# Kernel tuning notes

Measured on AMD Instinct MI355X. Metric: run time of the kernel, lower is better.

The kernel has to match this reference:

```python
import jax, jax.numpy as jnp
import numpy as np

DIM = 64; N_LAYER = 2; B = 2048; M = 64
N_ENT = 100000; N_REL = 200
TEMP = 0.2; KGE_W = 1e-6
MIN_N = 1e-15; BND = 1e-5


def _norm(x):
    return jnp.sqrt(jnp.clip((x * x).sum(-1, keepdims=True), MIN_N))


def _l2(x):
    # F.normalize(p=2): x / max(||x||, 1e-12)
    return x / jnp.maximum(jnp.sqrt((x * x).sum(-1, keepdims=True)), 1e-12)


def _artanh(x):
    return jnp.arctanh(jnp.clip(x, -1.0 + BND, 1.0 - BND))


def expmap0(u):
    n = _norm(u)
    return jnp.tanh(n) * u / n


def logmap0(x):
    n = _norm(x)
    return _artanh(n) * x / n


def mobius_add(x, y):
    x2 = (x * x).sum(-1, keepdims=True)
    y2 = (y * y).sum(-1, keepdims=True)
    xy = (x * y).sum(-1, keepdims=True)
    num = (1 + 2 * xy + y2) * x + (1 - x2) * y
    den = 1 + 2 * xy + x2 * y2
    return num / jnp.clip(den, MIN_N)


def expmap(u, p):
    lam = 2.0 / jnp.clip(1.0 - (p * p).sum(-1, keepdims=True), MIN_N)
    n = _norm(u)
    return mobius_add(p, jnp.tanh(lam * n / 2.0) * u / n)


def logmap(x, p):
    m = mobius_add(-p, x)
    n = _norm(m)
    lam = 2.0 / jnp.clip(1.0 - (p * p).sum(-1, keepdims=True), MIN_N)
    return (2.0 / lam) * _artanh(n) * m / n


def _ed_agg(h, path, t, att_w1, att_w2):
    # attention: Linear(2d,d,no bias) -> LeakyReLU(0)==ReLU -> Linear(d,1,no bias) -> Sigmoid
    x = jnp.concatenate([h, path], -1)                       # [B,M,2d]
    a = jax.nn.sigmoid(jax.nn.relu(x @ att_w1) @ att_w2)[..., 0]  # [B,M]
    w = jax.nn.softmax(a, axis=-1)
    return (w[..., None] * t).sum(1)                          # [B,d]


def _hyper_agg(h, path, t, curvature, a2_w1, a2_b1, a2_w2, a2_b2):
    h, path, t = _l2(h), _l2(path), _l2(t)
    hh = expmap0(h) * jnp.abs(curvature)
    ht = expmap(t, hh)
    hr = expmap(path, hh)
    tang = logmap0(jnp.concatenate([hh, hr], -1))            # [B,M,2d]
    a = jnp.tanh(jax.nn.relu(tang @ a2_w1 + a2_b1) @ a2_w2 + a2_b2)[..., 0]
    w = jax.nn.softmax(a, axis=-1)                            # [B,M]
    agg = w[..., None] * ht
    mean_pt = (w[..., None] * hh).sum(1, keepdims=True)       # [B,1,d]
    e = logmap(agg, mean_pt)
    return (w[..., None] * e).sum(1)                          # [B,d]


def _build(E, R, h_idx, r_idx, t_idx, init_emb, agg):
    embs = [init_emb]
    for i in range(N_LAYER):
        h = E[h_idx[0]]
        path = R[r_idx[0]]
        for k in range(1, i + 1):  # faithful to source: inner loop reuses index i
            h = h + E[h_idx[i]]
            path = path * R[r_idx[i]]
        embs.append(agg(h, path, E[t_idx[i]]))
    return jnp.stack(embs)  # [L+1, B, d]


def _mlcl(a_stack, b_stack):
    # vectorized over layer index i of MLCL_Loss(a[i], b[i], a_list, b_list)
    na, nb = _l2(a_stack), _l2(b_stack)                       # [L+1,B,d]
    d = na.shape[-1]
    pos = (na * nb).sum(-1)                                   # [L+1,B]
    ttl1 = jnp.einsum('lbd,md->lbm', na, nb.reshape(-1, d))
    ttl2 = jnp.einsum('lbd,md->lbm', nb, na.reshape(-1, d))
    ep = jnp.exp(pos / TEMP)
    l1 = -jnp.log(ep / jnp.exp(ttl1 / TEMP).sum(-1)).sum()
    l2 = -jnp.log(ep / jnp.exp(ttl2 / TEMP).sum(-1)).sum()
    return KGE_W * (l1 + l2)


def _cat_rev(stack):
    # e = stack[0]; for i in 1..L: e = cat(stack[i], e) -> [L, L-1, ..., 0]
    return jnp.concatenate([stack[i] for i in range(stack.shape[0] - 1, -1, -1)], -1)


def setup_inputs() -> dict:
    key = jax.random.key(0)
    ks = jax.random.split(key, 24)
    def ent_idx(k):
        return jax.random.randint(k, (N_LAYER, B, M), 0, N_ENT, dtype=jnp.int32)
    def rel_idx(k):
        return jax.random.randint(k, (N_LAYER, B, M), 0, N_REL, dtype=jnp.int32)
    inp = {
        'items': jax.random.randint(ks[0], (B,), 0, N_ENT, dtype=jnp.int32),
        'ucf_h': ent_idx(ks[1]), 'ucf_r': rel_idx(ks[2]), 'ucf_t': ent_idx(ks[3]),
        'ikg_h': ent_idx(ks[4]), 'ikg_r': rel_idx(ks[5]), 'ikg_t': ent_idx(ks[6]),
        'ukg_h': ent_idx(ks[7]), 'ukg_r': rel_idx(ks[8]), 'ukg_t': ent_idx(ks[9]),
        'icf_h': ent_idx(ks[10]), 'icf_r': rel_idx(ks[11]), 'icf_t': ent_idx(ks[12]),
        'ent_emb': jax.random.normal(ks[13], (N_ENT, DIM), jnp.float32) * 0.02,
        'rel_emb': jax.random.normal(ks[14], (N_REL, DIM), jnp.float32) * 0.02,
        'att_w1': jax.random.normal(ks[15], (2 * DIM, DIM), jnp.float32) * 0.05,
        'att_w2': jax.random.normal(ks[16], (DIM, 1), jnp.float32) * 0.05,
        'att2_w1': jax.random.normal(ks[17], (2 * DIM, DIM), jnp.float32) * 0.05,
        'att2_b1': jnp.zeros((DIM,), jnp.float32),
        'att2_w2': jax.random.normal(ks[18], (DIM, 1), jnp.float32) * 0.05,
        'att2_b2': jnp.zeros((1,), jnp.float32),
        'curvature': jnp.asarray(1.0, jnp.float32),
    }
    return inp


def reference(items, ucf_h, ucf_r, ucf_t, ikg_h, ikg_r, ikg_t,
              ukg_h, ukg_r, ukg_t, icf_h, icf_r, icf_t,
              ent_emb, rel_emb, att_w1, att_w2,
              att2_w1, att2_b1, att2_w2, att2_b2, curvature):
    ed = lambda h, p, t: _ed_agg(h, p, t, att_w1, att_w2)
    hy = lambda h, p, t: _hyper_agg(h, p, t, curvature, att2_w1, att2_b1, att2_w2, att2_b2)
    ucf = _build(ent_emb, rel_emb, ucf_h, ucf_r, ucf_t, ent_emb[ucf_h[0]].mean(1), ed)
    ikg = _build(ent_emb, rel_emb, ikg_h, ikg_r, ikg_t, ent_emb[items], ed)
    ukg = _build(ent_emb, rel_emb, ukg_h, ukg_r, ukg_t, ent_emb[ukg_h[0]].mean(1), hy)
    icf = _build(ent_emb, rel_emb, icf_h, icf_r, icf_t, ent_emb[icf_h[0]].mean(1), hy)
    kge_loss = _mlcl(ucf, ukg) + _mlcl(ikg, icf)
    e_u = jnp.concatenate([_cat_rev(ucf), _cat_rev(ukg)], -1)
    e_i = jnp.concatenate([_cat_rev(icf), _cat_rev(ikg)], -1)
    scores = jax.nn.sigmoid((e_i * e_u).sum(-1))
    return scores, kge_loss
```

## Files before the change

kernel.cpp:

```cpp
#include <hip/hip_runtime.h>
#include <hip/hip_bf16.h>
#include <cstdint>
#include <cstddef>

constexpr int NB = 2048;
constexpr int NM = 64;
constexpr int ND = 64;
constexpr int NBM = NB * NM;
constexpr int NROWS = 3 * NB;
constexpr int STACK = 3 * NB * ND;
constexpr int NZ = 8;

typedef __attribute__((ext_vector_type(8))) short short8;
typedef __attribute__((ext_vector_type(4))) float float4v;

__device__ __forceinline__ float wsum(float v) {
#pragma unroll
  for (int o = 32; o > 0; o >>= 1) v += __shfl_xor(v, o, 64);
  return v;
}

__device__ __forceinline__ float wmax(float v) {
#pragma unroll
  for (int o = 32; o > 0; o >>= 1) v = fmaxf(v, __shfl_xor(v, o, 64));
  return v;
}

__device__ __forceinline__ float rcpf(float x) { return __builtin_amdgcn_rcpf(x); }
__device__ __forceinline__ float sqf(float x) { return __builtin_amdgcn_sqrtf(x); }

__device__ __forceinline__ float fast_tanh(float x) {
  float t = __expf(2.f * x);
  return (t - 1.f) * rcpf(t + 1.f);
}

__device__ __forceinline__ float artanh_clip(float x) {
  x = fminf(fmaxf(x, -1.f + 1e-5f), 1.f - 1e-5f);
  return 0.5f * __logf((1.f + x) * rcpf(1.f - x));
}

__device__ __forceinline__ ushort f2bf(float f) {
  return (ushort)((__float_as_uint(f) + 0x8000u) >> 16);
}
__device__ __forceinline__ float bf2f(ushort u) {
  return __uint_as_float((uint)u << 16);
}
__device__ __forceinline__ uint pack_bf2(float h, float p) {
  uint hu = __float_as_uint(h) + 0x8000u;
  uint pu = __float_as_uint(p) + 0x8000u;
  return __builtin_amdgcn_perm(pu, hu, 0x07060302);
}
__device__ __forceinline__ float hp_lo(uint v) { return __uint_as_float(v << 16); }
__device__ __forceinline__ float hp_hi(uint v) { return __uint_as_float(v & 0xFFFF0000u); }

__device__ __forceinline__ float readlane_f(float v, int l) {
  return __int_as_float(__builtin_amdgcn_readlane(__float_as_int(v), l));
}

__device__ __forceinline__ void write_row_norm(
    float v, float* __restrict__ frow, ushort* __restrict__ nstack,
    int r, int lane) {
  float nv = wsum(v * v);
  float rr = rcpf(fmaxf(sqf(nv), 1e-12f));
  frow[lane] = v;
  int q = (lane >> 3) & 3, half = lane >> 5, j = lane & 7;
  int fl = (r & 15) | (q << 4);
  nstack[(size_t)(r >> 4) * 1024 + fl * 16 + half * 8 + j] = f2bf(v * rr);
}

__global__ __launch_bounds__(64) void prep_kernel(
    const float* __restrict__ E, const int* __restrict__ items,
    const float* __restrict__ w1_ed, const float* __restrict__ w1_hy,
    float* __restrict__ s_ikg, ushort* __restrict__ nbf_ikg,
    ushort* __restrict__ w1p_ed, ushort* __restrict__ w1p_hy) {
  int blk = blockIdx.x, lane = threadIdx.x;
  if (blk < NB) {
    float v = E[(size_t)items[blk] * ND + lane];
    write_row_norm(v, s_ikg + (size_t)blk * ND, nbf_ikg, blk, lane);
  } else {
    int e = (blk - NB) * 64 + lane;
    const float* w1 = (e < 8192) ? w1_ed : w1_hy;
    ushort* out = (e < 8192) ? w1p_ed : w1p_hy;
    e &= 8191;
    int j = e & 7, ln = (e >> 3) & 63, nt = (e >> 9) & 3, kt = e >> 11;
    int n = nt * 16 + (ln & 15), k = kt * 32 + ((ln >> 4) << 3) + j;
    out[e] = f2bf(w1[k * 64 + n]);
  }
}

constexpr int OFF_H = 0;
constexpr int OFF_P = 4608;
constexpr int OFF_T = 9728;
constexpr int XS = 152;
constexpr int REGA_SZ = 14336;

__global__ __launch_bounds__(256) void agg_all_kernel(
    const float* __restrict__ E, const float* __restrict__ R,
    const int* __restrict__ h0, const int* __restrict__ r0, const int* __restrict__ t0,
    const int* __restrict__ h1, const int* __restrict__ r1, const int* __restrict__ t1,
    const int* __restrict__ h2, const int* __restrict__ r2, const int* __restrict__ t2,
    const int* __restrict__ h3, const int* __restrict__ r3, const int* __restrict__ t3,
    const ushort* __restrict__ w1p_ed, const float* __restrict__ w2_ed,
    const ushort* __restrict__ w1p_hy, const float* __restrict__ b1,
    const float* __restrict__ w2_hy, const float* __restrict__ b2,
    const float* __restrict__ curv,
    float* __restrict__ stacks, ushort* __restrict__ nbf) {
  __shared__ __align__(16) ushort regA[REGA_SZ];
  __shared__ float a_s[64];
  __shared__ float part[4][64];
  __shared__ float minit[4][64];

  const int b = blockIdx.x;
  const int fam = blockIdx.y;
  const int tid = threadIdx.x;
  const int wave = tid >> 6, lane = tid & 63;
  const int m0 = __builtin_amdgcn_readfirstlane(wave) * 16;
  const int colq = lane & 15, quad = lane >> 4;
  const size_t L = (size_t)NB * ND;

  const int* h_idx = (fam == 0) ? h0 : (fam == 1) ? h1 : (fam == 2) ? h2 : h3;
  const int* r_idx = (fam == 0) ? r0 : (fam == 1) ? r1 : (fam == 2) ? r2 : r3;
  const int* t_idx = (fam == 0) ? t0 : (fam == 1) ? t1 : (fam == 2) ? t2 : t3;
  float* sb = stacks + (size_t)fam * STACK;
  ushort* nb = nbf + (size_t)fam * STACK;

  uint hp[16];

  if (fam < 2) {
    const int do_init = (fam == 0);
    for (int layer = 0; layer < 2; ++layer) {
      float tv[16];
      if (layer == 0) {
        float macc = 0.f;
#pragma unroll
        for (int mi = 0; mi < 16; ++mi) {
          const int m = m0 + mi;
          float hd = E[(size_t)h_idx[b * NM + m] * ND + lane];
          float pd = R[(size_t)r_idx[b * NM + m] * ND + lane];
          macc += hd;
          uint pk = pack_bf2(hd, pd);
          hp[mi] = pk;
          regA[m * XS + lane] = (ushort)pk;
          regA[m * XS + 64 + lane] = (ushort)(pk >> 16);
        }
        if (do_init) minit[wave][lane] = macc;
      } else {
#pragma unroll
        for (int mi = 0; mi < 16; ++mi) {
          const int m = m0 + mi;
          float hd = hp_lo(hp[mi]) + E[(size_t)h_idx[NBM + b * NM + m] * ND + lane];
          float pd = hp_hi(hp[mi]) * R[(size_t)r_idx[NBM + b * NM + m] * ND + lane];
          uint pk = pack_bf2(hd, pd);
          hp[mi] = pk;
          regA[m * XS + lane] = (ushort)pk;
          regA[m * XS + 64 + lane] = (ushort)(pk >> 16);
        }
      }
#pragma unroll
      for (int mi = 0; mi < 16; ++mi)
        tv[mi] = E[(size_t)t_idx[(size_t)layer * NBM + b * NM + m0 + mi] * ND + lane];

      {
        short8 afr[4];
#pragma unroll
        for (int kt = 0; kt < 4; ++kt)
          afr[kt] = *(const short8*)&regA[(m0 + colq) * XS + kt * 32 + quad * 8];
        float w2v[4];
#pragma unroll
        for (int nt = 0; nt < 4; ++nt) w2v[nt] = w2_ed[nt * 16 + colq];
        float cc[4][4];
#pragma unroll
        for (int nt = 0; nt < 4; ++nt) {
          float4v c = {0.f, 0.f, 0.f, 0.f};
#pragma unroll
          for (int kt = 0; kt < 4; ++kt) {
            short8 bfr = *(const short8*)&w1p_ed[(((kt << 2) | nt) * 64 + lane) * 8];
            c = __builtin_amdgcn_mfma_f32_16x16x32_bf16(afr[kt], bfr, c, 0, 0, 0);
          }
#pragma unroll
          for (int i = 0; i < 4; ++i) cc[nt][i] = c[i];
        }
        float sred[4];
#pragma unroll
        for (int i = 0; i < 4; ++i)
          sred[i] = fmaxf(cc[0][i], 0.f) * w2v[0] + fmaxf(cc[1][i], 0.f) * w2v[1] +
                    fmaxf(cc[2][i], 0.f) * w2v[2] + fmaxf(cc[3][i], 0.f) * w2v[3];
#pragma unroll
        for (int o = 8; o > 0; o >>= 1) {
#pragma unroll
          for (int i = 0; i < 4; ++i) sred[i] += __shfl_xor(sred[i], o, 64);
        }
        if (colq == 0) {
#pragma unroll
          for (int i = 0; i < 4; ++i)
            a_s[m0 + quad * 4 + i] = 1.f / (1.f + __expf(-sred[i]));
        }
      }
      __syncthreads();

      float wl;
      {
        float v = a_s[lane];
        float mx = wmax(v);
        float e = __expf(v - mx);
        wl = e / wsum(e);
      }
      if (layer == 0 && do_init && wave == 0) {
        float v = (minit[0][lane] + minit[1][lane] + minit[2][lane] + minit[3][lane]) * (1.f / 64.f);
        write_row_norm(v, sb + (size_t)b * ND, nb, b, lane);
      }

      float o = 0.f;
#pragma unroll
      for (int mi = 0; mi < 16; ++mi)
        o = fmaf(readlane_f(wl, m0 + mi), tv[mi], o);
      part[wave][lane] = o;
      __syncthreads();
      if (wave == 0) {
        float v = part[0][lane] + part[1][lane] + part[2][lane] + part[3][lane];
        write_row_norm(v, sb + (layer + 1) * L + (size_t)b * ND,
                       nb, (layer + 1) * NB + b, lane);
      }
    }
  } else {
    const float cabs = fabsf(*curv);
    const int j = colq;
    const int srcl = ((j >> 2) << 4) + j;

    for (int layer = 0; layer < 2; ++layer) {
      if (layer == 0) {
        float macc = 0.f;
#pragma unroll
        for (int mi = 0; mi < 16; ++mi) {
          const int m = m0 + mi;
          float hd = E[(size_t)h_idx[b * NM + m] * ND + lane];
          float pd = R[(size_t)r_idx[b * NM + m] * ND + lane];
          float td = E[(size_t)t_idx[b * NM + m] * ND + lane];
          macc += hd;
          uint pk = pack_bf2(hd, pd);
          hp[mi] = pk;
          regA[OFF_H + m * 72 + lane] = (ushort)pk;
          regA[OFF_P + m * 72 + lane] = (ushort)(pk >> 16);
          regA[OFF_T + m * 72 + lane] = f2bf(td);
        }
        part[wave][lane] = macc;
      } else {
#pragma unroll
        for (int mi = 0; mi < 16; ++mi) {
          const int m = m0 + mi;
          float hd = hp_lo(hp[mi]) + E[(size_t)h_idx[NBM + b * NM + m] * ND + lane];
          float pd = hp_hi(hp[mi]) * R[(size_t)r_idx[NBM + b * NM + m] * ND + lane];
          float td = E[(size_t)t_idx[(size_t)NBM + b * NM + m] * ND + lane];
          uint pk = pack_bf2(hd, pd);
          hp[mi] = pk;
          regA[OFF_H + m * 72 + lane] = (ushort)pk;
          regA[OFF_P + m * 72 + lane] = (ushort)(pk >> 16);
          regA[OFF_T + m * 72 + lane] = f2bf(td);
        }
      }

      float sh, sp, st, sht, shp;
      {
        const int fr = m0 + colq;
        const ushort* pH = &regA[OFF_H + fr * 72 + quad * 8];
        const ushort* pP = &regA[OFF_P + fr * 72 + quad * 8];
        const ushort* pT = &regA[OFF_T + fr * 72 + quad * 8];
        short8 hh0 = *(const short8*)pH, hh1 = *(const short8*)(pH + 32);
        short8 pp0 = *(const short8*)pP, pp1 = *(const short8*)(pP + 32);
        short8 tt0 = *(const short8*)pT, tt1 = *(const short8*)(pT + 32);
        const int dr = colq & 3;
#define DIAG_DOT(OUTV, A0, A1, B0, B1)                                      \
        {                                                                    \
          float4v c = {0.f, 0.f, 0.f, 0.f};                                  \
          c = __builtin_amdgcn_mfma_f32_16x16x32_bf16(A0, B0, c, 0, 0, 0);   \
          c = __builtin_amdgcn_mfma_f32_16x16x32_bf16(A1, B1, c, 0, 0, 0);   \
          float dv = (dr & 2) ? ((dr & 1) ? c[3] : c[2])                     \
                              : ((dr & 1) ? c[1] : c[0]);                    \
          OUTV = __shfl(dv, srcl, 64);                                       \
        }
        DIAG_DOT(sh, hh0, hh1, hh0, hh1)
        DIAG_DOT(sp, pp0, pp1, pp0, pp1)
        DIAG_DOT(st, tt0, tt1, tt0, tt1)
        DIAG_DOT(sht, hh0, hh1, tt0, tt1)
        DIAG_DOT(shp, hh0, hh1, pp0, pp1)
#undef DIAG_DOT
      }

      float g_ch, g_e1, g_e2, g_gh, g_q1, g_q2, g_hts2;
      {
        float rih = rcpf(fmaxf(sqf(sh), 1e-12f));
        float rip = rcpf(fmaxf(sqf(sp), 1e-12f));
        float rit = rcpf(fmaxf(sqf(st), 1e-12f));
        float nh = sqf(fmaxf(sh * rih * rih, 1e-15f));
        float ch = fast_tanh(nh) * rcpf(nh) * rih * cabs;
        float p2 = ch * ch * sh;
        float lam = 2.f * rcpf(fmaxf(1.f - p2, 1e-15f));
        float ntn = sqf(fmaxf(st * rit * rit, 1e-15f));
        float ct = fast_tanh(0.5f * lam * ntn) * rcpf(ntn) * rit;
        float y2 = ct * ct * st, xy = ch * ct * sht;
        float At = 1.f + 2.f * xy + y2, Bt = 1.f - p2;
        float rdt = rcpf(fmaxf(1.f + 2.f * xy + p2 * y2, 1e-15f));
        g_e1 = At * ch * rdt;
        g_e2 = Bt * ct * rdt;
        g_hts2 = g_e1 * g_e1 * sh + 2.f * g_e1 * g_e2 * sht + g_e2 * g_e2 * st;
        float npn = sqf(fmaxf(sp * rip * rip, 1e-15f));
        float cp = fast_tanh(0.5f * lam * npn) * rcpf(npn) * rip;
        float z2 = cp * cp * sp, xz = ch * cp * shp;
        float Ar = 1.f + 2.f * xz + z2;
        float rdr = rcpf(fmaxf(1.f + 2.f * xz + p2 * z2, 1e-15f));
        float f1 = Ar * ch * rdr, f2 = Bt * cp * rdr;
        float hr2 = f1 * f1 * sh + 2.f * f1 * f2 * shp + f2 * f2 * sp;
        float n128 = sqf(fmaxf(p2 + hr2, 1e-15f));
        float fq = artanh_clip(n128) * rcpf(n128);
        g_ch = ch;
        g_gh = fq * ch;
        g_q1 = fq * f1;
        g_q2 = fq * f2;
      }

      __syncthreads();
      if (layer == 0 && wave == 0) {
        float v = (part[0][lane] + part[1][lane] + part[2][lane] + part[3][lane]) * (1.f / 64.f);
        write_row_norm(v, sb + (size_t)b * ND, nb, b, lane);
      }

#pragma unroll
      for (int mi = 0; mi < 16; ++mi) {
        const int m = m0 + mi;
        float hvf = hp_lo(hp[mi]);
        float pvf = hp_hi(hp[mi]);
        float tvf = bf2f(regA[OFF_T + m * 72 + lane]);
        float ghm = readlane_f(g_gh, mi);
        float q1m = readlane_f(g_q1, mi);
        float q2m = readlane_f(g_q2, mi);
        float e1m = readlane_f(g_e1, mi);
        float e2m = readlane_f(g_e2, mi);
        regA[m * XS + lane] = f2bf(ghm * hvf);
        regA[m * XS + 64 + lane] = f2bf(q1m * hvf + q2m * pvf);
        regA[OFF_T + m * 72 + lane] = f2bf(e1m * hvf + e2m * tvf);
      }

      {
        short8 afr[4];
#pragma unroll
        for (int kt = 0; kt < 4; ++kt)
          afr[kt] = *(const short8*)&regA[(m0 + colq) * XS + kt * 32 + quad * 8];
        float b1v[4], w2v[4];
#pragma unroll
        for (int nt = 0; nt < 4; ++nt) {
          b1v[nt] = b1[nt * 16 + colq];
          w2v[nt] = w2_hy[nt * 16 + colq];
        }
        float cc[4][4];
#pragma unroll
        for (int nt = 0; nt < 4; ++nt) {
          float4v c = {0.f, 0.f, 0.f, 0.f};
#pragma unroll
          for (int kt = 0; kt < 4; ++kt) {
            short8 bfr = *(const short8*)&w1p_hy[(((kt << 2) | nt) * 64 + lane) * 8];
            c = __builtin_amdgcn_mfma_f32_16x16x32_bf16(afr[kt], bfr, c, 0, 0, 0);
          }
#pragma unroll
          for (int i = 0; i < 4; ++i) cc[nt][i] = c[i];
        }
        float b2v = b2[0];
        float sred[4];
#pragma unroll
        for (int i = 0; i < 4; ++i)
          sred[i] = fmaxf(cc[0][i] + b1v[0], 0.f) * w2v[0] +
                    fmaxf(cc[1][i] + b1v[1], 0.f) * w2v[1] +
                    fmaxf(cc[2][i] + b1v[2], 0.f) * w2v[2] +
                    fmaxf(cc[3][i] + b1v[3], 0.f) * w2v[3];
#pragma unroll
        for (int o = 8; o > 0; o >>= 1) {
#pragma unroll
          for (int i = 0; i < 4; ++i) sred[i] += __shfl_xor(sred[i], o, 64);
        }
        if (colq == 0) {
#pragma unroll
          for (int i = 0; i < 4; ++i)
            a_s[m0 + quad * 4 + i] = fast_tanh(sred[i] + b2v);
        }
      }
      __syncthreads();

      float wl;
      {
        float v = a_s[lane];
        float mx = wmax(v);
        float e = __expf(v - mx);
        wl = e / wsum(e);
      }

      float mp = 0.f;
#pragma unroll
      for (int mi = 0; mi < 16; ++mi)
        mp = fmaf(readlane_f(wl, m0 + mi) * readlane_f(g_ch, mi), hp_lo(hp[mi]), mp);
      part[wave][lane] = mp;
      __syncthreads();

      float mv = part[0][lane] + part[1][lane] + part[2][lane] + part[3][lane];
      float p2m = wsum(mv * mv);

      float dpv;
      {
        const ushort* pA = &regA[OFF_T + (m0 + colq) * 72 + quad * 8];
        short8 a0 = *(const short8*)pA, a1 = *(const short8*)(pA + 32);
        short8 bm0, bm1;
#pragma unroll
        for (int jj = 0; jj < 8; ++jj) {
          bm0[jj] = (short)f2bf(__shfl(mv, quad * 8 + jj, 64));
          bm1[jj] = (short)f2bf(__shfl(mv, 32 + quad * 8 + jj, 64));
        }
        float4v c = {0.f, 0.f, 0.f, 0.f};
        c = __builtin_amdgcn_mfma_f32_16x16x32_bf16(a0, bm0, c, 0, 0, 0);
        c = __builtin_amdgcn_mfma_f32_16x16x32_bf16(a1, bm1, c, 0, 0, 0);
        const int dr = colq & 3;
        float dv = (dr & 2) ? ((dr & 1) ? c[3] : c[2]) : ((dr & 1) ? c[1] : c[0]);
        dpv = __shfl(dv, srcl, 64);
      }

      const float be = fmaxf(1.f - p2m, 1e-15f);
      float g1, g2;
      {
        float wm = __shfl(wl, m0 + j, 64);
        float y2 = wm * wm * g_hts2;
        float xy = -wm * dpv;
        float al = 1.f + 2.f * xy + y2;
        float rd = rcpf(fmaxf(1.f + 2.f * xy + p2m * y2, 1e-15f));
        float md2 = (al * al * p2m - 2.f * al * be * wm * dpv + be * be * y2) * rd * rd;
        float n = sqf(fmaxf(md2, 1e-15f));
        float sm = be * artanh_clip(n) * rcpf(n) * rd;
        g1 = wm * wm * sm * be;
        g2 = wm * sm * al;
      }
      float ovec = 0.f, cA = 0.f;
#pragma unroll
      for (int mi = 0; mi < 16; ++mi) {
        const int m = m0 + mi;
        float htf = bf2f(regA[OFF_T + m * 72 + lane]);
        ovec = fmaf(readlane_f(g1, mi), htf, ovec);
        cA += readlane_f(g2, mi);
      }
      part[wave][lane] = ovec - cA * mv;
      __syncthreads();
      if (wave == 0) {
        float v = part[0][lane] + part[1][lane] + part[2][lane] + part[3][lane];
        write_row_norm(v, sb + (layer + 1) * L + (size_t)b * ND,
                       nb, (layer + 1) * NB + b, lane);
      }
    }
  }
}

__global__ __launch_bounds__(256) void pos_scores_kernel(
    const ushort* __restrict__ nbf, const float* __restrict__ stacks,
    float* __restrict__ pos, float* __restrict__ out) {
  int lane = threadIdx.x & 63;
  int wave = threadIdx.x >> 6;
  if (blockIdx.y < 2) {
    if (blockIdx.x >= 96) return;
    int g = blockIdx.x * 4 + wave;
    int sa = blockIdx.y;
    const ushort* X = nbf + (size_t)sa * STACK + (size_t)g * 1024 + lane * 16;
    const ushort* Yp = nbf + (size_t)(sa + 2) * STACK + (size_t)g * 1024 + lane * 16;
    short8 x0 = *(const short8*)X, x1 = *(const short8*)(X + 8);
    short8 y0 = *(const short8*)Yp, y1 = *(const short8*)(Yp + 8);
    float d = 0.f;
#pragma unroll
    for (int jj = 0; jj < 8; ++jj)
      d += bf2f((ushort)x0[jj]) * bf2f((ushort)y0[jj]) +
           bf2f((ushort)x1[jj]) * bf2f((ushort)y1[jj]);
    d += __shfl_xor(d, 16, 64);
    d += __shfl_xor(d, 32, 64);
    if (lane < 16) pos[sa * NROWS + g * 16 + lane] = d;
  } else {
    int b = blockIdx.x * 4 + wave;
    if (b >= NB) return;
    float s = 0.f;
#pragma unroll
    for (int l = 0; l < 3; ++l) {
      size_t o = (size_t)l * NB * ND + (size_t)b * ND + lane;
      s += stacks[0 * (size_t)STACK + o] * stacks[3 * (size_t)STACK + o]
         + stacks[2 * (size_t)STACK + o] * stacks[1 * (size_t)STACK + o];
    }
    s = wsum(s);
    if (lane == 0) out[b] = 1.f / (1.f + __expf(-s));
  }
}

__global__ __launch_bounds__(256) void lse_mfma_kernel(
    const ushort* __restrict__ nbf, float* __restrict__ Spart) {
  const int tid = threadIdx.x;
  const int wave = tid >> 6, lane = tid & 63;
  const int pair = blockIdx.y;
  const int z = blockIdx.z;
  int xi = (pair & 2) ? ((pair & 1) ? 3 : 1) : ((pair & 1) ? 2 : 0);
  int yi = xi ^ 2;
  const ushort* X = nbf + (size_t)xi * STACK;
  const ushort* Y = nbf + (size_t)yi * STACK;
  const int r0 = blockIdx.x * 64 + wave * 16;
  const int g = r0 >> 4;
  const int row = lane & 15, quad = lane >> 4;
  (void)quad;

  short8 a0 = *(const short8*)&X[(size_t)g * 1024 + lane * 16];
  short8 a1 = *(const short8*)&X[(size_t)g * 1024 + lane * 16 + 8];

  float rsum[4] = {0.f, 0.f, 0.f, 0.f};
  const int cg0 = z * (NROWS / NZ / 16);
  for (int ct = 0; ct < NROWS / NZ / 16; ++ct) {
    const ushort* yp = &Y[(size_t)(cg0 + ct) * 1024 + lane * 16];
    short8 b0 = *(const short8*)yp;
    short8 b1 = *(const short8*)(yp + 8);
    float4v c = {0.f, 0.f, 0.f, 0.f};
    c = __builtin_amdgcn_mfma_f32_16x16x32_bf16(a0, b0, c, 0, 0, 0);
    c = __builtin_amdgcn_mfma_f32_16x16x32_bf16(a1, b1, c, 0, 0, 0);
#pragma unroll
    for (int i = 0; i < 4; ++i) rsum[i] += __expf(c[i] * 5.f);
  }
#pragma unroll
  for (int i = 0; i < 4; ++i) {
    float v = rsum[i];
    v += __shfl_xor(v, 1, 64);
    v += __shfl_xor(v, 2, 64);
    v += __shfl_xor(v, 4, 64);
    v += __shfl_xor(v, 8, 64);
    if (row == 0)
      Spart[((size_t)z * 4 + pair) * NROWS + r0 + (lane >> 4) * 4 + i] = v;
  }
}

__global__ __launch_bounds__(256) void loss_part_kernel(
    const float* __restrict__ Spart, const float* __restrict__ pos,
    double* __restrict__ lossp) {
  __shared__ double red[256];
  const int t = threadIdx.x, blk = blockIdx.x;
  double acc = 0.0;
#pragma unroll
  for (int r = 0; r < 2; ++r) {
    int i = blk * 512 + r * 256 + t;
    float s = 0.f;
#pragma unroll
    for (int zz = 0; zz < NZ; ++zz) s += Spart[i + zz * 4 * NROWS];
    acc += (double)__logf(s);
  }
  {
    int jj = blk * 256 + t;
    acc -= 10.0 * (double)pos[jj];
  }
  red[t] = acc;
  __syncthreads();
  for (int s = 128; s > 0; s >>= 1) {
    if (t < s) red[t] += red[t + s];
    __syncthreads();
  }
  if (t == 0) lossp[blk] = red[0];
}

__global__ __launch_bounds__(64) void loss_final_kernel(
    const double* __restrict__ lossp, float* __restrict__ out) {
  int lane = threadIdx.x;
  double v = (lane < 48) ? lossp[lane] : 0.0;
#pragma unroll
  for (int o = 32; o > 0; o >>= 1) v += __shfl_xor(v, o, 64);
  if (lane == 0) out[NB] = (float)(1e-6 * v);
}

extern "C" void kernel_launch(void* const* d_in, const int* in_sizes, int n_in,
                              void* d_out, int out_size, void* d_ws, size_t ws_size,
                              hipStream_t stream) {
  const int* items = (const int*)d_in[0];
  const int* ucf_h = (const int*)d_in[1];
  const int* ucf_r = (const int*)d_in[2];
  const int* ucf_t = (const int*)d_in[3];
  const int* ikg_h = (const int*)d_in[4];
  const int* ikg_r = (const int*)d_in[5];
  const int* ikg_t = (const int*)d_in[6];
  const int* ukg_h = (const int*)d_in[7];
  const int* ukg_r = (const int*)d_in[8];
  const int* ukg_t = (const int*)d_in[9];
  const int* icf_h = (const int*)d_in[10];
  const int* icf_r = (const int*)d_in[11];
  const int* icf_t = (const int*)d_in[12];
  const float* E = (const float*)d_in[13];
  const float* R = (const float*)d_in[14];
  const float* att_w1 = (const float*)d_in[15];
  const float* att_w2 = (const float*)d_in[16];
  const float* a2_w1 = (const float*)d_in[17];
  const float* a2_b1 = (const float*)d_in[18];
  const float* a2_w2 = (const float*)d_in[19];
  const float* a2_b2 = (const float*)d_in[20];
  const float* curv = (const float*)d_in[21];
  float* outp = (float*)d_out;

  float* ws = (float*)d_ws;
  float* stacks = ws;
  float* Spart = stacks + 4 * (size_t)STACK;
  float* posarr = Spart + (size_t)NZ * 4 * NROWS;
  ushort* nbf = (ushort*)(posarr + 2 * (size_t)NROWS);
  ushort* w1p_ed = nbf + 4 * (size_t)STACK;
  ushort* w1p_hy = w1p_ed + 8192;
  double* lossp = (double*)(w1p_hy + 8192);

  float* ikg = stacks + 1 * (size_t)STACK;
  ushort* nbf_ikg = nbf + 1 * (size_t)STACK;

  prep_kernel<<<NB + 256, 64, 0, stream>>>(E, items, att_w1, a2_w1,
                                           ikg, nbf_ikg, w1p_ed, w1p_hy);

  agg_all_kernel<<<dim3(NB, 4), 256, 0, stream>>>(
      E, R,
      ucf_h, ucf_r, ucf_t, ikg_h, ikg_r, ikg_t,
      ukg_h, ukg_r, ukg_t, icf_h, icf_r, icf_t,
      w1p_ed, att_w2, w1p_hy, a2_b1, a2_w2, a2_b2, curv,
      stacks, nbf);

  pos_scores_kernel<<<dim3(NB / 4, 3), 256, 0, stream>>>(nbf, stacks, posarr, outp);
  lse_mfma_kernel<<<dim3(NROWS / 64, 4, NZ), 256, 0, stream>>>(nbf, Spart);

  loss_part_kernel<<<48, 256, 0, stream>>>(Spart, posarr, lossp);
  loss_final_kernel<<<1, 64, 0, stream>>>(lossp, outp);
}
```

Before: 385.3 us.

## Write normalized rows row-major and relayout to MFMA fragments in separate kernel

The aggregation kernel now stores each normalized bf16 row contiguously instead of scattering it into the MFMA fragment layout. A new relayout kernel copies these rows into a separate fragment-ordered buffer, which the LSE MFMA kernel reads. The positive-pair dot kernel is rewritten to use the row-major copy with one wave per row and a full wave reduction. The aim is simpler, coalesced stores in the main kernel, at the cost of an extra launch, an extra workspace buffer and one more pass over the bf16 stacks.

```diff
diff --git a/kernel.cpp b/kernel.cpp
--- a/kernel.cpp
+++ b/kernel.cpp
@@ -58,14 +58,11 @@
 }
 
 __device__ __forceinline__ void write_row_norm(
-    float v, float* __restrict__ frow, ushort* __restrict__ nstack,
-    int r, int lane) {
+    float v, float* __restrict__ frow, ushort* __restrict__ nrow, int lane) {
   float nv = wsum(v * v);
-  float rr = rcpf(fmaxf(sqf(nv), 1e-12f));
+  float r = rcpf(fmaxf(sqf(nv), 1e-12f));
   frow[lane] = v;
-  int q = (lane >> 3) & 3, half = lane >> 5, j = lane & 7;
-  int fl = (r & 15) | (q << 4);
-  nstack[(size_t)(r >> 4) * 1024 + fl * 16 + half * 8 + j] = f2bf(v * rr);
+  nrow[lane] = f2bf(v * r);
 }
 
 __global__ __launch_bounds__(64) void prep_kernel(
@@ -76,7 +73,7 @@
   int blk = blockIdx.x, lane = threadIdx.x;
   if (blk < NB) {
     float v = E[(size_t)items[blk] * ND + lane];
-    write_row_norm(v, s_ikg + (size_t)blk * ND, nbf_ikg, blk, lane);
+    write_row_norm(v, s_ikg + (size_t)blk * ND, nbf_ikg + (size_t)blk * ND, lane);
   } else {
     int e = (blk - NB) * 64 + lane;
     const float* w1 = (e < 8192) ? w1_ed : w1_hy;
@@ -207,7 +204,7 @@
       }
       if (layer == 0 && do_init && wave == 0) {
         float v = (minit[0][lane] + minit[1][lane] + minit[2][lane] + minit[3][lane]) * (1.f / 64.f);
-        write_row_norm(v, sb + (size_t)b * ND, nb, b, lane);
+        write_row_norm(v, sb + (size_t)b * ND, nb + (size_t)b * ND, lane);
       }
 
       float o = 0.f;
@@ -219,7 +216,7 @@
       if (wave == 0) {
         float v = part[0][lane] + part[1][lane] + part[2][lane] + part[3][lane];
         write_row_norm(v, sb + (layer + 1) * L + (size_t)b * ND,
-                       nb, (layer + 1) * NB + b, lane);
+                       nb + (layer + 1) * L + (size_t)b * ND, lane);
       }
     }
   } else {
@@ -321,7 +318,7 @@
       __syncthreads();
       if (layer == 0 && wave == 0) {
         float v = (part[0][lane] + part[1][lane] + part[2][lane] + part[3][lane]) * (1.f / 64.f);
-        write_row_norm(v, sb + (size_t)b * ND, nb, b, lane);
+        write_row_norm(v, sb + (size_t)b * ND, nb + (size_t)b * ND, lane);
       }
 
 #pragma unroll
@@ -447,10 +444,22 @@
       if (wave == 0) {
         float v = part[0][lane] + part[1][lane] + part[2][lane] + part[3][lane];
         write_row_norm(v, sb + (layer + 1) * L + (size_t)b * ND,
-                       nb, (layer + 1) * NB + b, lane);
+                       nb + (layer + 1) * L + (size_t)b * ND, lane);
       }
     }
   }
+}
+
+__global__ __launch_bounds__(256) void relayout_kernel(
+    const ushort* __restrict__ nbf, ushort* __restrict__ nbfF) {
+  int lane = threadIdx.x & 63;
+  int wave = threadIdx.x >> 6;
+  int g = blockIdx.x * 4 + wave;
+  int s = blockIdx.y;
+  const ushort* src = nbf + (size_t)s * STACK + (size_t)(g * 16 + (lane & 15)) * ND + (lane >> 4) * 8;
+  ushort* dst = nbfF + (size_t)s * STACK + (size_t)g * 1024 + lane * 16;
+  *(short8*)dst = *(const short8*)src;
+  *(short8*)(dst + 8) = *(const short8*)(src + 32);
 }
 
 __global__ __launch_bounds__(256) void pos_scores_kernel(
@@ -459,21 +468,12 @@
   int lane = threadIdx.x & 63;
   int wave = threadIdx.x >> 6;
   if (blockIdx.y < 2) {
-    if (blockIdx.x >= 96) return;
-    int g = blockIdx.x * 4 + wave;
+    int row = blockIdx.x * 4 + wave;
     int sa = blockIdx.y;
-    const ushort* X = nbf + (size_t)sa * STACK + (size_t)g * 1024 + lane * 16;
-    const ushort* Yp = nbf + (size_t)(sa + 2) * STACK + (size_t)g * 1024 + lane * 16;
-    short8 x0 = *(const short8*)X, x1 = *(const short8*)(X + 8);
-    short8 y0 = *(const short8*)Yp, y1 = *(const short8*)(Yp + 8);
-    float d = 0.f;
-#pragma unroll
-    for (int jj = 0; jj < 8; ++jj)
-      d += bf2f((ushort)x0[jj]) * bf2f((ushort)y0[jj]) +
-           bf2f((ushort)x1[jj]) * bf2f((ushort)y1[jj]);
-    d += __shfl_xor(d, 16, 64);
-    d += __shfl_xor(d, 32, 64);
-    if (lane < 16) pos[sa * NROWS + g * 16 + lane] = d;
+    float a = bf2f(nbf[(size_t)sa * STACK + (size_t)row * ND + lane]);
+    float c = bf2f(nbf[(size_t)(sa + 2) * STACK + (size_t)row * ND + lane]);
+    float d = wsum(a * c);
+    if (lane == 0) pos[sa * NROWS + row] = d;
   } else {
     int b = blockIdx.x * 4 + wave;
     if (b >= NB) return;
@@ -490,19 +490,18 @@
 }
 
 __global__ __launch_bounds__(256) void lse_mfma_kernel(
-    const ushort* __restrict__ nbf, float* __restrict__ Spart) {
+    const ushort* __restrict__ nbfF, float* __restrict__ Spart) {
   const int tid = threadIdx.x;
   const int wave = tid >> 6, lane = tid & 63;
   const int pair = blockIdx.y;
   const int z = blockIdx.z;
   int xi = (pair & 2) ? ((pair & 1) ? 3 : 1) : ((pair & 1) ? 2 : 0);
   int yi = xi ^ 2;
-  const ushort* X = nbf + (size_t)xi * STACK;
-  const ushort* Y = nbf + (size_t)yi * STACK;
+  const ushort* X = nbfF + (size_t)xi * STACK;
+  const ushort* Y = nbfF + (size_t)yi * STACK;
   const int r0 = blockIdx.x * 64 + wave * 16;
   const int g = r0 >> 4;
-  const int row = lane & 15, quad = lane >> 4;
-  (void)quad;
+  const int row = lane & 15;
 
   short8 a0 = *(const short8*)&X[(size_t)g * 1024 + lane * 16];
   short8 a1 = *(const short8*)&X[(size_t)g * 1024 + lane * 16 + 8];
@@ -599,7 +598,8 @@
   float* Spart = stacks + 4 * (size_t)STACK;
   float* posarr = Spart + (size_t)NZ * 4 * NROWS;
   ushort* nbf = (ushort*)(posarr + 2 * (size_t)NROWS);
-  ushort* w1p_ed = nbf + 4 * (size_t)STACK;
+  ushort* nbfF = nbf + 4 * (size_t)STACK;
+  ushort* w1p_ed = nbfF + 4 * (size_t)STACK;
   ushort* w1p_hy = w1p_ed + 8192;
   double* lossp = (double*)(w1p_hy + 8192);
 
@@ -616,8 +616,9 @@
       w1p_ed, att_w2, w1p_hy, a2_b1, a2_w2, a2_b2, curv,
       stacks, nbf);
 
-  pos_scores_kernel<<<dim3(NB / 4, 3), 256, 0, stream>>>(nbf, stacks, posarr, outp);
-  lse_mfma_kernel<<<dim3(NROWS / 64, 4, NZ), 256, 0, stream>>>(nbf, Spart);
+  relayout_kernel<<<dim3(96, 4), 256, 0, stream>>>(nbf, nbfF);
+  pos_scores_kernel<<<dim3(NROWS / 4, 3), 256, 0, stream>>>(nbf, stacks, posarr, outp);
+  lse_mfma_kernel<<<dim3(NROWS / 64, 4, NZ), 256, 0, stream>>>(nbfF, Spart);
 
   loss_part_kernel<<<48, 256, 0, stream>>>(Spart, posarr, lossp);
   loss_final_kernel<<<1, 64, 0, stream>>>(lossp, outp);
```

Result: faster. 347.1 us (-9.9%).
